# Kernel optimization log

Hardware: AMD Instinct MI355X
Metric: run time of the kernel (lower is better)

## Reference

```python
import jax, jax.numpy as jnp
import numpy as np

N, C = 16384, 2048
CPG = 16          # num_pergroup (c)
T = 5             # Newton-Schulz iterations
EPS = 1e-5


def setup_inputs() -> dict:
    key = jax.random.key(0)
    k1, k2, k3 = jax.random.split(key, 3)
    return {
        "x": jax.random.normal(k1, (N, C), dtype=jnp.float32),
        "sw_mean_weight": jax.random.normal(k2, (2,), dtype=jnp.float32),
        "sw_var_weight": jax.random.normal(k3, (2,), dtype=jnp.float32),
        "weight": jnp.ones((C,), dtype=jnp.float32),
        "bias": jnp.zeros((C,), dtype=jnp.float32),
    }


def reference(x, sw_mean_weight, sw_var_weight, weight, bias):
    n, ch = x.shape
    c = CPG
    g = ch // c
    # --- BW (batch whitening) stats: x.T viewed as (g, c, N) ---
    xt = x.T.reshape(g, c, n)
    mean_bn = jnp.mean(xt, axis=-1, keepdims=True)            # (g, c, 1)
    xc = xt - mean_bn
    cov_bn = jnp.einsum('gcn,gdn->gcd', xc, xc) / n           # (g, c, c)
    # --- IW stats: in_data = x.view(N*g, c, 1) => mean_in = in_data, cov_in = 0 ---
    mw = jax.nn.softmax(sw_mean_weight)
    vw = jax.nn.softmax(sw_var_weight)
    eye = jnp.eye(c, dtype=x.dtype)
    # cov identical for every sample (cov_in == 0) -> whiten once per group
    cov = vw[0] * cov_bn + EPS * eye                          # (g, c, c)
    # --- Newton-Schulz iterative whitening ---
    rTr = 1.0 / jnp.trace(cov, axis1=1, axis2=2)[:, None, None]
    covN = cov * rTr
    P = jnp.broadcast_to(eye, (g, c, c))
    for _ in range(T):
        P3 = jnp.einsum('gab,gbc,gcd->gad', P, P, P)
        P = 1.5 * P - 0.5 * jnp.einsum('gad,gde->gae', P3, covN)
    wm = P * jnp.sqrt(rTr)                                    # (g, c, c)
    # --- apply: wm @ (in_data - mean),  mean = mw0*mean_bn + mw1*in_data ---
    z = x.reshape(n, g, c)
    zc = (1.0 - mw[1]) * z - mw[0] * mean_bn[None, :, :, 0]   # (N, g, c)
    y = jnp.einsum('gcd,ngd->ngc', wm, zc).reshape(n, ch)
    return y * weight + bias
```

## Files before the change

kernel.cpp:

```cpp
#include <hip/hip_runtime.h>
#include <cstddef>

typedef float f4 __attribute__((ext_vector_type(4)));

#define NROWS 16384
#define NCOLS 2048
#define NGRP  128
#define EPS_W 1e-5f
#define NS_T  5

#define TROWS 32
#define S_CH  128
#define S_RPB (NROWS / S_CH)
#define S_NT  (S_RPB / TROWS)
#define PART_STRIDE 272

#define A_STRIPES 256
#define A_RPB (NROWS / A_STRIPES)

__global__ __launch_bounds__(256) void k_stats(const float* __restrict__ x,
                                               float* __restrict__ part) {
  __shared__ __align__(16) float tile[TROWS * 256];
  const int cb   = blockIdx.x;
  const int ch   = blockIdx.y;
  const int t    = threadIdx.x;
  const int col0 = cb << 8;
  const int r0   = ch * S_RPB;

  const int g  = t >> 4;
  const int ti = t & 15;
  const int tc = (ti >> 2) << 2;
  const int td = (ti & 3) << 2;

  float mac = 0.f;
  float acc[4][4] = {{0.f}};

  f4 st[8];
#pragma unroll
  for (int i = 0; i < 8; ++i) {
    const int f = (i << 8) | t;
    const int r = f >> 6, cq = f & 63;
    st[i] = *(const f4*)(x + (size_t)(r0 + r) * NCOLS + col0 + (cq << 2));
  }

  for (int tb = 0; tb < S_NT; ++tb) {
    __syncthreads();
#pragma unroll
    for (int i = 0; i < 8; ++i) {
      const int f = (i << 8) | t;
      *(f4*)(&tile[f << 2]) = st[i];
    }
    __syncthreads();
    if (tb + 1 < S_NT) {
      const int rn = r0 + (tb + 1) * TROWS;
#pragma unroll
      for (int i = 0; i < 8; ++i) {
        const int f = (i << 8) | t;
        const int r = f >> 6, cq = f & 63;
        st[i] = *(const f4*)(x + (size_t)(rn + r) * NCOLS + col0 + (cq << 2));
      }
    }
#pragma unroll 4
    for (int r = 0; r < TROWS; ++r) {
      const float* row = tile + r * 256;
      mac += row[t];
      const f4 xa = *(const f4*)(row + (g << 4) + tc);
      const f4 xb = *(const f4*)(row + (g << 4) + td);
#pragma unroll
      for (int i = 0; i < 4; ++i)
#pragma unroll
        for (int j = 0; j < 4; ++j)
          acc[i][j] += xa[i] * xb[j];
    }
  }

  float* pg = part + (size_t)((cb << 4) + g) * PART_STRIDE;
  atomicAdd(&pg[ti], mac);
#pragma unroll
  for (int i = 0; i < 4; ++i)
#pragma unroll
    for (int j = 0; j < 4; ++j)
      atomicAdd(&pg[16 + (tc + i) * 16 + (td + j)], acc[i][j]);
}

__global__ __launch_bounds__(256) void k_ns(const float* __restrict__ part,
                                            const float* __restrict__ swm,
                                            const float* __restrict__ swv,
                                            const float* __restrict__ wgt,
                                            const float* __restrict__ bia,
                                            float* __restrict__ A2,
                                            float* __restrict__ b2) {
  __shared__ float sP[256], sA[256], sB[256], sN[256], smean[16];
  __shared__ float strace;
  const int G = blockIdx.x;
  const int t = threadIdx.x;
  const int c = t >> 4, d = t & 15;

  const float m2 = part[(size_t)G * PART_STRIDE + 16 + t];
  if (t < 16) smean[t] = part[(size_t)G * PART_STRIDE + t] * (1.f / NROWS);
  __syncthreads();

  const float a0 = swm[0], a1 = swm[1];
  const float am = fmaxf(a0, a1);
  const float e0 = expf(a0 - am), e1 = expf(a1 - am);
  const float mw0 = e0 / (e0 + e1), mw1 = e1 / (e0 + e1);
  const float v0 = swv[0], v1 = swv[1];
  const float vm = fmaxf(v0, v1);
  const float f0 = expf(v0 - vm), f1 = expf(v1 - vm);
  const float vw0 = f0 / (f0 + f1);

  float cov = m2 * (1.f / NROWS) - smean[c] * smean[d];
  cov = vw0 * cov + ((c == d) ? EPS_W : 0.f);
  sN[t] = cov;
  __syncthreads();
  if (t == 0) {
    float tr = 0.f;
#pragma unroll
    for (int k = 0; k < 16; ++k) tr += sN[k * 17];
    strace = 1.f / tr;
  }
  __syncthreads();
  const float rTr = strace;
  sN[t] = cov * rTr;
  sP[t] = (c == d) ? 1.f : 0.f;
  __syncthreads();

  for (int it = 0; it < NS_T; ++it) {
    float p2 = 0.f;
#pragma unroll
    for (int k = 0; k < 16; ++k) p2 += sP[c * 16 + k] * sP[k * 16 + d];
    sA[t] = p2;
    __syncthreads();
    float p3 = 0.f;
#pragma unroll
    for (int k = 0; k < 16; ++k) p3 += sA[c * 16 + k] * sP[k * 16 + d];
    sB[t] = p3;
    __syncthreads();
    float qv = 0.f;
#pragma unroll
    for (int k = 0; k < 16; ++k) qv += sB[c * 16 + k] * sN[k * 16 + d];
    const float np = 1.5f * sP[t] - 0.5f * qv;
    __syncthreads();
    sP[t] = np;
    __syncthreads();
  }

  const float wmv = sP[t] * sqrtf(rTr);
  const float wr = wgt[(G << 4) + c];
  A2[(size_t)G * 256 + t] = wmv * (1.f - mw1) * wr;
  sA[t] = wmv * smean[d];
  __syncthreads();
  if (t < 16) {
    float s = 0.f;
#pragma unroll
    for (int k = 0; k < 16; ++k) s += sA[t * 16 + k];
    b2[(G << 4) + t] = -mw0 * s * wgt[(G << 4) + t] + bia[(G << 4) + t];
  }
}

__device__ __forceinline__ float dot16(const f4* ar, f4 u0, f4 u1, f4 u2, f4 u3) {
  const f4 p = ar[0] * u0 + ar[1] * u1 + ar[2] * u2 + ar[3] * u3;
  return p.x + p.y + p.z + p.w;
}

__global__ __launch_bounds__(256) void k_apply(const float* __restrict__ x,
                                               const float* __restrict__ A2,
                                               const float* __restrict__ b2,
                                               float* __restrict__ y) {
  const int cb  = blockIdx.x;
  const int stb = blockIdx.y;
  const int t   = threadIdx.x;
  const int q   = t & 3;
  const int g   = (t >> 2) & 15;
  const int ph  = t >> 6;
  const int G   = (cb << 4) | g;
  const int col0 = cb << 8;

  f4 a[4][4];
#pragma unroll
  for (int i = 0; i < 4; ++i)
#pragma unroll
    for (int dq = 0; dq < 4; ++dq)
      a[i][dq] = *(const f4*)(A2 + (size_t)G * 256 + ((q << 2) + i) * 16 + (dq << 2));
  const f4 bv = *(const f4*)(b2 + (G << 4) + (q << 2));

  const int r0 = stb * A_RPB + ph;
  const size_t xoff = (size_t)col0 + (g << 4);
  const size_t yoff = (size_t)col0 + ((size_t)(t & 63) << 2);

  for (int i = 0; i < A_RPB / 4; i += 2) {
    const size_t ra = (size_t)(r0 + 4 * i) * NCOLS;
    const size_t rb = (size_t)(r0 + 4 * i + 4) * NCOLS;
    const float* pa = x + ra + xoff;
    const float* pb = x + rb + xoff;
    const f4 u0 = __builtin_nontemporal_load((const f4*)(pa + 0));
    const f4 u1 = __builtin_nontemporal_load((const f4*)(pa + 4));
    const f4 u2 = __builtin_nontemporal_load((const f4*)(pa + 8));
    const f4 u3 = __builtin_nontemporal_load((const f4*)(pa + 12));
    const f4 v0 = __builtin_nontemporal_load((const f4*)(pb + 0));
    const f4 v1 = __builtin_nontemporal_load((const f4*)(pb + 4));
    const f4 v2 = __builtin_nontemporal_load((const f4*)(pb + 8));
    const f4 v3 = __builtin_nontemporal_load((const f4*)(pb + 12));

    f4 oa, ob;
    oa.x = bv.x + dot16(a[0], u0, u1, u2, u3);
    oa.y = bv.y + dot16(a[1], u0, u1, u2, u3);
    oa.z = bv.z + dot16(a[2], u0, u1, u2, u3);
    oa.w = bv.w + dot16(a[3], u0, u1, u2, u3);
    __builtin_nontemporal_store(oa, (f4*)(y + ra + yoff));
    ob.x = bv.x + dot16(a[0], v0, v1, v2, v3);
    ob.y = bv.y + dot16(a[1], v0, v1, v2, v3);
    ob.z = bv.z + dot16(a[2], v0, v1, v2, v3);
    ob.w = bv.w + dot16(a[3], v0, v1, v2, v3);
    __builtin_nontemporal_store(ob, (f4*)(y + rb + yoff));
  }
}

extern "C" void kernel_launch(void* const* d_in, const int* in_sizes, int n_in,
                              void* d_out, int out_size, void* d_ws, size_t ws_size,
                              hipStream_t stream) {
  (void)in_sizes; (void)n_in; (void)out_size; (void)ws_size;
  const float* x   = (const float*)d_in[0];
  const float* swm = (const float*)d_in[1];
  const float* swv = (const float*)d_in[2];
  const float* wgt = (const float*)d_in[3];
  const float* bia = (const float*)d_in[4];
  float* out = (float*)d_out;

  float* part = (float*)d_ws;
  float* A2   = part + (size_t)NGRP * PART_STRIDE;
  float* b2   = A2 + (size_t)NGRP * 256;

  hipMemsetAsync(part, 0, (size_t)NGRP * PART_STRIDE * sizeof(float), stream);
  k_stats<<<dim3(8, S_CH), 256, 0, stream>>>(x, part);
  k_ns<<<NGRP, 256, 0, stream>>>(part, swm, swv, wgt, bia, A2, b2);
  k_apply<<<dim3(8, A_STRIPES), 256, 0, stream>>>(x, A2, b2, out);
}
```

Measured before the change: 362.0 us.

## Restructure stats kernel to register-direct loads with shuffle reduction and per-chunk partials

The stats kernel stops staging tiles in shared memory. Each thread loads its group's columns straight into registers with software prefetch, reduces across lanes with shuffles, and writes per-chunk partial sums instead of using atomics, so the memset goes away. The NS kernel now sums the 32 partials, and the apply kernel gains register double-buffered prefetch. The aim is to remove LDS traffic, atomic contention and the memset, at the cost of more registers and fewer, larger blocks (256 blocks of 512 threads).

```diff
diff --git a/kernel.cpp b/kernel.cpp
--- a/kernel.cpp
+++ b/kernel.cpp
@@ -8,79 +8,114 @@
 #define NGRP  128
 #define EPS_W 1e-5f
 #define NS_T  5
-
-#define TROWS 32
-#define S_CH  128
+#define PART_STRIDE 272
+
+#define S_CH 32
 #define S_RPB (NROWS / S_CH)
-#define S_NT  (S_RPB / TROWS)
-#define PART_STRIDE 272
+#define S_HROWS (S_RPB / 2)
+#define S_STEPS (S_HROWS / 4)
 
 #define A_STRIPES 256
 #define A_RPB (NROWS / A_STRIPES)
 
-__global__ __launch_bounds__(256) void k_stats(const float* __restrict__ x,
+__device__ __forceinline__ f4 sxor(f4 v, int m) {
+  f4 r;
+  r.x = __shfl_xor(v.x, m, 64);
+  r.y = __shfl_xor(v.y, m, 64);
+  r.z = __shfl_xor(v.z, m, 64);
+  r.w = __shfl_xor(v.w, m, 64);
+  return r;
+}
+
+__global__ __launch_bounds__(512) void k_stats(const float* __restrict__ x,
                                                float* __restrict__ part) {
-  __shared__ __align__(16) float tile[TROWS * 256];
-  const int cb   = blockIdx.x;
-  const int ch   = blockIdx.y;
-  const int t    = threadIdx.x;
+  __shared__ float red[64 * 72];
+  const int t  = threadIdx.x;
+  const int cb = blockIdx.x;
+  const int ch = blockIdx.y;
+  const int g  = t & 15;
+  const int p  = (t >> 4) & 3;
+  const int tc = (t >> 6) & 3;
+  const int h  = t >> 8;
   const int col0 = cb << 8;
-  const int r0   = ch * S_RPB;
-
-  const int g  = t >> 4;
-  const int ti = t & 15;
-  const int tc = (ti >> 2) << 2;
-  const int td = (ti & 3) << 2;
-
-  float mac = 0.f;
-  float acc[4][4] = {{0.f}};
-
-  f4 st[8];
-#pragma unroll
-  for (int i = 0; i < 8; ++i) {
-    const int f = (i << 8) | t;
-    const int r = f >> 6, cq = f & 63;
-    st[i] = *(const f4*)(x + (size_t)(r0 + r) * NCOLS + col0 + (cq << 2));
-  }
-
-  for (int tb = 0; tb < S_NT; ++tb) {
-    __syncthreads();
-#pragma unroll
-    for (int i = 0; i < 8; ++i) {
-      const int f = (i << 8) | t;
-      *(f4*)(&tile[f << 2]) = st[i];
-    }
-    __syncthreads();
-    if (tb + 1 < S_NT) {
-      const int rn = r0 + (tb + 1) * TROWS;
-#pragma unroll
-      for (int i = 0; i < 8; ++i) {
-        const int f = (i << 8) | t;
-        const int r = f >> 6, cq = f & 63;
-        st[i] = *(const f4*)(x + (size_t)(rn + r) * NCOLS + col0 + (cq << 2));
-      }
-    }
-#pragma unroll 4
-    for (int r = 0; r < TROWS; ++r) {
-      const float* row = tile + r * 256;
-      mac += row[t];
-      const f4 xa = *(const f4*)(row + (g << 4) + tc);
-      const f4 xb = *(const f4*)(row + (g << 4) + td);
-#pragma unroll
-      for (int i = 0; i < 4; ++i)
-#pragma unroll
-        for (int j = 0; j < 4; ++j)
-          acc[i][j] += xa[i] * xb[j];
-    }
-  }
-
-  float* pg = part + (size_t)((cb << 4) + g) * PART_STRIDE;
-  atomicAdd(&pg[ti], mac);
+
+  const size_t rbase = (size_t)ch * S_RPB + (size_t)h * S_HROWS + p;
+  const float* bp = x + rbase * NCOLS + col0 + (g << 4);
+  const size_t stp = (size_t)4 * NCOLS;
+
+  const f4 zero = {0.f, 0.f, 0.f, 0.f};
+  f4 acc[4][4];
 #pragma unroll
   for (int i = 0; i < 4; ++i)
 #pragma unroll
-    for (int j = 0; j < 4; ++j)
-      atomicAdd(&pg[16 + (tc + i) * 16 + (td + j)], acc[i][j]);
+    for (int j = 0; j < 4; ++j) acc[i][j] = zero;
+  f4 macc = zero;
+
+  f4 q0, q1, q2, q3, xa, n0, n1, n2, n3, nx;
+  q0 = *(const f4*)(bp + 0);
+  q1 = *(const f4*)(bp + 4);
+  q2 = *(const f4*)(bp + 8);
+  q3 = *(const f4*)(bp + 12);
+  xa = *(const f4*)(bp + (tc << 2));
+
+  for (int s = 0; s < S_STEPS; ++s) {
+    if (s + 1 < S_STEPS) {
+      const float* pn = bp + (size_t)(s + 1) * stp;
+      n0 = *(const f4*)(pn + 0);
+      n1 = *(const f4*)(pn + 4);
+      n2 = *(const f4*)(pn + 8);
+      n3 = *(const f4*)(pn + 12);
+      nx = *(const f4*)(pn + (tc << 2));
+    }
+    macc += xa;
+#pragma unroll
+    for (int i = 0; i < 4; ++i) {
+      const float sc = xa[i];
+      acc[i][0] += sc * q0;
+      acc[i][1] += sc * q1;
+      acc[i][2] += sc * q2;
+      acc[i][3] += sc * q3;
+    }
+    q0 = n0; q1 = n1; q2 = n2; q3 = n3; xa = nx;
+    if ((s & 7) == 7) __syncthreads();
+  }
+
+#pragma unroll
+  for (int i = 0; i < 4; ++i)
+#pragma unroll
+    for (int j = 0; j < 4; ++j) {
+      acc[i][j] += sxor(acc[i][j], 16);
+      acc[i][j] += sxor(acc[i][j], 32);
+    }
+  macc += sxor(macc, 16);
+  macc += sxor(macc, 32);
+
+  const int slot = ((tc << 4) | g) * 72;
+  if (h == 1 && p == 0) {
+    *(f4*)&red[slot] = macc;
+#pragma unroll
+    for (int i = 0; i < 4; ++i)
+#pragma unroll
+      for (int j = 0; j < 4; ++j)
+        *(f4*)&red[slot + 4 + i * 16 + (j << 2)] = acc[i][j];
+  }
+  __syncthreads();
+  if (h == 0 && p == 0) {
+    macc += *(const f4*)&red[slot];
+#pragma unroll
+    for (int i = 0; i < 4; ++i)
+#pragma unroll
+      for (int j = 0; j < 4; ++j)
+        acc[i][j] += *(const f4*)&red[slot + 4 + i * 16 + (j << 2)];
+
+    float* pg = part + ((size_t)ch * NGRP + (cb << 4) + g) * PART_STRIDE;
+    *(f4*)(pg + (tc << 2)) = macc;
+#pragma unroll
+    for (int i = 0; i < 4; ++i)
+#pragma unroll
+      for (int j = 0; j < 4; ++j)
+        *(f4*)(pg + 16 + (tc << 6) + i * 16 + (j << 2)) = acc[i][j];
+  }
 }
 
 __global__ __launch_bounds__(256) void k_ns(const float* __restrict__ part,
@@ -90,14 +125,31 @@
                                             const float* __restrict__ bia,
                                             float* __restrict__ A2,
                                             float* __restrict__ b2) {
+  __shared__ float sred[272];
   __shared__ float sP[256], sA[256], sB[256], sN[256], smean[16];
   __shared__ float strace;
   const int G = blockIdx.x;
   const int t = threadIdx.x;
   const int c = t >> 4, d = t & 15;
 
-  const float m2 = part[(size_t)G * PART_STRIDE + 16 + t];
-  if (t < 16) smean[t] = part[(size_t)G * PART_STRIDE + t] * (1.f / NROWS);
+  {
+    float s0 = 0.f;
+#pragma unroll 4
+    for (int ch = 0; ch < S_CH; ++ch)
+      s0 += part[((size_t)ch * NGRP + G) * PART_STRIDE + t];
+    sred[t] = s0;
+    if (t < 16) {
+      float s1 = 0.f;
+#pragma unroll 4
+      for (int ch = 0; ch < S_CH; ++ch)
+        s1 += part[((size_t)ch * NGRP + G) * PART_STRIDE + 256 + t];
+      sred[256 + t] = s1;
+    }
+  }
+  __syncthreads();
+
+  const float m2 = sred[16 + t];
+  if (t < 16) smean[t] = sred[t] * (1.f / NROWS);
   __syncthreads();
 
   const float a0 = swm[0], a1 = swm[1];
@@ -162,6 +214,12 @@
   const f4 p = ar[0] * u0 + ar[1] * u1 + ar[2] * u2 + ar[3] * u3;
   return p.x + p.y + p.z + p.w;
 }
+
+#define LDP(P, A0, A1, A2_, A3)                                   \
+  A0 = __builtin_nontemporal_load((const f4*)((P) + 0));          \
+  A1 = __builtin_nontemporal_load((const f4*)((P) + 4));          \
+  A2_ = __builtin_nontemporal_load((const f4*)((P) + 8));         \
+  A3 = __builtin_nontemporal_load((const f4*)((P) + 12));
 
 __global__ __launch_bounds__(256) void k_apply(const float* __restrict__ x,
                                                const float* __restrict__ A2,
@@ -188,20 +246,20 @@
   const size_t xoff = (size_t)col0 + (g << 4);
   const size_t yoff = (size_t)col0 + ((size_t)(t & 63) << 2);
 
-  for (int i = 0; i < A_RPB / 4; i += 2) {
-    const size_t ra = (size_t)(r0 + 4 * i) * NCOLS;
-    const size_t rb = (size_t)(r0 + 4 * i + 4) * NCOLS;
-    const float* pa = x + ra + xoff;
-    const float* pb = x + rb + xoff;
-    const f4 u0 = __builtin_nontemporal_load((const f4*)(pa + 0));
-    const f4 u1 = __builtin_nontemporal_load((const f4*)(pa + 4));
-    const f4 u2 = __builtin_nontemporal_load((const f4*)(pa + 8));
-    const f4 u3 = __builtin_nontemporal_load((const f4*)(pa + 12));
-    const f4 v0 = __builtin_nontemporal_load((const f4*)(pb + 0));
-    const f4 v1 = __builtin_nontemporal_load((const f4*)(pb + 4));
-    const f4 v2 = __builtin_nontemporal_load((const f4*)(pb + 8));
-    const f4 v3 = __builtin_nontemporal_load((const f4*)(pb + 12));
-
+  const float* pa = x + (size_t)r0 * NCOLS + xoff;
+
+  f4 u0, u1, u2, u3, v0, v1, v2, v3;
+  f4 m0, m1, m2, m3, w0, w1, w2, w3;
+  LDP(pa, u0, u1, u2, u3)
+  LDP(pa + (size_t)4 * NCOLS, v0, v1, v2, v3)
+
+  for (int s = 0; s < A_RPB / 8; ++s) {
+    if (s + 1 < A_RPB / 8) {
+      const float* pn = pa + (size_t)(s + 1) * 8 * NCOLS;
+      LDP(pn, m0, m1, m2, m3)
+      LDP(pn + (size_t)4 * NCOLS, w0, w1, w2, w3)
+    }
+    const size_t ra = (size_t)(r0 + 8 * s) * NCOLS;
     f4 oa, ob;
     oa.x = bv.x + dot16(a[0], u0, u1, u2, u3);
     oa.y = bv.y + dot16(a[1], u0, u1, u2, u3);
@@ -212,7 +270,9 @@
     ob.y = bv.y + dot16(a[1], v0, v1, v2, v3);
     ob.z = bv.z + dot16(a[2], v0, v1, v2, v3);
     ob.w = bv.w + dot16(a[3], v0, v1, v2, v3);
-    __builtin_nontemporal_store(ob, (f4*)(y + rb + yoff));
+    __builtin_nontemporal_store(ob, (f4*)(y + ra + (size_t)4 * NCOLS + yoff));
+    u0 = m0; u1 = m1; u2 = m2; u3 = m3;
+    v0 = w0; v1 = w1; v2 = w2; v3 = w3;
   }
 }
 
@@ -228,11 +288,10 @@
   float* out = (float*)d_out;
 
   float* part = (float*)d_ws;
-  float* A2   = part + (size_t)NGRP * PART_STRIDE;
+  float* A2   = part + (size_t)S_CH * NGRP * PART_STRIDE;
   float* b2   = A2 + (size_t)NGRP * 256;
 
-  hipMemsetAsync(part, 0, (size_t)NGRP * PART_STRIDE * sizeof(float), stream);
-  k_stats<<<dim3(8, S_CH), 256, 0, stream>>>(x, part);
+  k_stats<<<dim3(8, S_CH), 512, 0, stream>>>(x, part);
   k_ns<<<NGRP, 256, 0, stream>>>(part, swm, swv, wgt, bia, A2, b2);
   k_apply<<<dim3(8, A_STRIPES), 256, 0, stream>>>(x, A2, b2, out);
 }
```

After: 305.4 us. 15.6% less time.
